# Kernel tuning notes

Hardware: AMD Instinct MI355X
Metric: run time of the kernel (lower is better)

## Reference

```python
import jax, jax.numpy as jnp
import numpy as np

N, NUM_CLASSES, FEAT_DIM = 32768, 395, 512


def setup_inputs() -> dict:
    key = jax.random.key(0)
    k1, k2, k3, k4 = jax.random.split(key, 4)
    modal1_inputs = jax.random.normal(k1, (N, FEAT_DIM), dtype=jnp.float32)
    modal2_inputs = jax.random.normal(k2, (N, FEAT_DIM), dtype=jnp.float32)
    targets = jax.random.randint(k3, (N,), 0, NUM_CLASSES)
    # learned centers parameter: torch.rand -> uniform [0, 1)
    centers = jax.random.uniform(k4, (NUM_CLASSES, FEAT_DIM), dtype=jnp.float32)
    return {
        "modal1_inputs": modal1_inputs,
        "modal2_inputs": modal2_inputs,
        "centers": centers,
        "targets": targets,
    }


def _smooth_l1(a, b):
    # SmoothL1Loss with default beta=1.0, reduction='mean'
    d = jnp.abs(a - b)
    return jnp.mean(jnp.where(d < 1.0, 0.5 * d * d, d - 0.5))


def reference(modal1_inputs, modal2_inputs, centers, targets):
    num_classes = centers.shape[0]
    # Per-label mean (the original O(N^2) loop is exactly a segment mean
    # gathered back per sample).
    ones = jnp.ones((targets.shape[0],), dtype=modal1_inputs.dtype)
    counts = jax.ops.segment_sum(ones, targets, num_segments=num_classes)
    counts = jnp.maximum(counts, 1.0)  # empty classes never gathered
    sum1 = jax.ops.segment_sum(modal1_inputs, targets, num_segments=num_classes)
    sum2 = jax.ops.segment_sum(modal2_inputs, targets, num_segments=num_classes)
    centersR = (sum1 / counts[:, None])[targets]  # [N, D]
    centersT = (sum2 / counts[:, None])[targets]  # [N, D]
    gathered_centers = centers[targets]           # [N, D]
    loss = _smooth_l1(centersR, gathered_centers) + _smooth_l1(centersT, gathered_centers)
    return loss
```

## Files before the change

kernel.cpp:

```cpp
#include <hip/hip_runtime.h>

#define NS 32768
#define NC 395
#define FD 512
#define SPLITS 4

__device__ int   g_hist[NC];
__device__ int   g_offs[NC];
__device__ int   g_cursor[NC];
__device__ float g_countsf[NC];
__device__ int   g_order[NS];
__device__ float g_partial[SPLITS * 2 * NC * FD];

__global__ void hist_scan_kernel(const int* __restrict__ targets,
                                 float* __restrict__ out) {
    __shared__ int lhist[NC];
    __shared__ int sc[512];
    int t = threadIdx.x;
    for (int i = t; i < NC; i += 1024) lhist[i] = 0;
    __syncthreads();
    for (int i = t; i < NS; i += 1024) atomicAdd(&lhist[targets[i]], 1);
    __syncthreads();
    if (t < 512) sc[t] = (t < NC) ? lhist[t] : 0;
    __syncthreads();
    for (int off = 1; off < 512; off <<= 1) {
        int v = 0;
        if (t < 512 && t >= off) v = sc[t - off];
        __syncthreads();
        if (t < 512) sc[t] += v;
        __syncthreads();
    }
    if (t < NC) {
        int cnt = lhist[t];
        int off = sc[t] - cnt;
        g_hist[t]    = cnt;
        g_offs[t]    = off;
        g_cursor[t]  = off;
        g_countsf[t] = (float)cnt;
    }
    if (t == 0) out[0] = 0.0f;
}

__global__ void scatter_kernel(const int* __restrict__ targets) {
    int i = blockIdx.x * blockDim.x + threadIdx.x;
    if (i < NS) {
        int pos = atomicAdd(&g_cursor[targets[i]], 1);
        g_order[pos] = i;
    }
}

__device__ __forceinline__ void f4add(float4& a, const float4 b) {
    a.x += b.x; a.y += b.y; a.z += b.z; a.w += b.w;
}

__global__ void gather_sum_kernel(const float4* __restrict__ m1,
                                  const float4* __restrict__ m2) {
    int c = blockIdx.x >> 2;
    int s = blockIdx.x & 3;
    int tid = threadIdx.x;
    int m = tid >> 7;
    int q = tid & 127;
    const float4* src = m ? m2 : m1;

    int start = g_offs[c];
    int n     = g_hist[c];
    int s0 = start + (n * s) / SPLITS;
    int s1 = start + (n * (s + 1)) / SPLITS;

    float4 a0 = make_float4(0.f, 0.f, 0.f, 0.f);
    float4 a1 = a0, a2 = a0, a3 = a0;

    __shared__ int sidx[256];
    for (int base = s0; base < s1; base += 256) {
        int nn = min(256, s1 - base);
        if (tid < nn) sidx[tid] = g_order[base + tid];
        __syncthreads();
        int j = 0;
        for (; j + 4 <= nn; j += 4) {
            int i0 = sidx[j], i1 = sidx[j + 1], i2 = sidx[j + 2], i3 = sidx[j + 3];
            float4 v0 = src[(size_t)i0 * 128 + q];
            float4 v1 = src[(size_t)i1 * 128 + q];
            float4 v2 = src[(size_t)i2 * 128 + q];
            float4 v3 = src[(size_t)i3 * 128 + q];
            f4add(a0, v0); f4add(a1, v1); f4add(a2, v2); f4add(a3, v3);
        }
        for (; j < nn; j++) {
            f4add(a0, src[(size_t)sidx[j] * 128 + q]);
        }
        __syncthreads();
    }
    f4add(a0, a1); f4add(a2, a3); f4add(a0, a2);

    float4* dst = reinterpret_cast<float4*>(g_partial);
    dst[(((size_t)s * 2 + m) * NC + c) * 128 + q] = a0;
}

__device__ __forceinline__ float smooth_l1(float d) {
    d = fabsf(d);
    return d < 1.0f ? 0.5f * d * d : d - 0.5f;
}

__global__ void loss_kernel(const float* __restrict__ centers,
                            float* __restrict__ out) {
    int gid = blockIdx.x * blockDim.x + threadIdx.x;
    float val = 0.0f;
    if (gid < NC * FD) {
        int c = gid >> 9;
        float cnt = g_countsf[c];
        if (cnt > 0.0f) {
            float sum1 = 0.0f, sum2 = 0.0f;
            #pragma unroll
            for (int s = 0; s < SPLITS; s++) {
                sum1 += g_partial[((s * 2 + 0) * NC) * FD + gid];
                sum2 += g_partial[((s * 2 + 1) * NC) * FD + gid];
            }
            float ctr = centers[gid];
            float inv = 1.0f / cnt;
            float f1 = smooth_l1(sum1 * inv - ctr);
            float f2 = smooth_l1(sum2 * inv - ctr);
            val = cnt * (f1 + f2);
        }
    }
    for (int off = 32; off > 0; off >>= 1)
        val += __shfl_down(val, off, 64);
    __shared__ float wsum[4];
    int lane = threadIdx.x & 63;
    int wid = threadIdx.x >> 6;
    if (lane == 0) wsum[wid] = val;
    __syncthreads();
    if (threadIdx.x == 0) {
        float s = wsum[0] + wsum[1] + wsum[2] + wsum[3];
        atomicAdd(out, s * 5.9604644775390625e-08f);
    }
}

extern "C" void kernel_launch(void* const* d_in, const int* in_sizes, int n_in,
                              void* d_out, int out_size, void* d_ws, size_t ws_size,
                              hipStream_t stream) {
    const float4* m1 = (const float4*)d_in[0];
    const float4* m2 = (const float4*)d_in[1];
    const float* centers = (const float*)d_in[2];
    const int* targets = (const int*)d_in[3];
    float* out = (float*)d_out;

    hist_scan_kernel<<<1, 1024, 0, stream>>>(targets, out);
    scatter_kernel<<<(NS + 255) / 256, 256, 0, stream>>>(targets);
    gather_sum_kernel<<<NC * SPLITS, 256, 0, stream>>>(m1, m2);
    loss_kernel<<<(NC * FD + 255) / 256, 256, 0, stream>>>(centers, out);
}
```

Measured before the change: 197.9 us.

## Parallelize histogram across blocks and double gather splits per class

The single-block histogram over all targets is split into a multi-block partial histogram kernel, followed by a separate scan kernel that sums the per-block partials and computes the class offsets. The gather-sum kernel now uses eight splits per class instead of four, putting more blocks in flight while the inputs are streamed. The cost is one extra kernel launch, a larger partial buffer, and more partial sums to read in the loss kernel.

```diff
diff --git a/kernel.cpp b/kernel.cpp
--- a/kernel.cpp
+++ b/kernel.cpp
@@ -3,8 +3,11 @@
 #define NS 32768
 #define NC 395
 #define FD 512
-#define SPLITS 4
+#define SPLITS 8
+#define HB 128
+#define HT 256
 
+__device__ int   g_hist_part[HB * NC];
 __device__ int   g_hist[NC];
 __device__ int   g_offs[NC];
 __device__ int   g_cursor[NC];
@@ -12,30 +15,37 @@
 __device__ int   g_order[NS];
 __device__ float g_partial[SPLITS * 2 * NC * FD];
 
-__global__ void hist_scan_kernel(const int* __restrict__ targets,
-                                 float* __restrict__ out) {
-    __shared__ int lhist[NC];
+__global__ void hist_kernel(const int* __restrict__ targets) {
+    __shared__ int lh[NC];
+    int t = threadIdx.x;
+    for (int i = t; i < NC; i += HT) lh[i] = 0;
+    __syncthreads();
+    atomicAdd(&lh[targets[blockIdx.x * HT + t]], 1);
+    __syncthreads();
+    int* slab = &g_hist_part[blockIdx.x * NC];
+    for (int c = t; c < NC; c += HT) slab[c] = lh[c];
+}
+
+__global__ void scan_kernel(float* __restrict__ out) {
     __shared__ int sc[512];
     int t = threadIdx.x;
-    for (int i = t; i < NC; i += 1024) lhist[i] = 0;
-    __syncthreads();
-    for (int i = t; i < NS; i += 1024) atomicAdd(&lhist[targets[i]], 1);
-    __syncthreads();
-    if (t < 512) sc[t] = (t < NC) ? lhist[t] : 0;
+    int cnt = 0;
+    if (t < NC) {
+        #pragma unroll 4
+        for (int p = 0; p < HB; p++) cnt += g_hist_part[p * NC + t];
+    }
+    sc[t] = (t < NC) ? cnt : 0;
     __syncthreads();
     for (int off = 1; off < 512; off <<= 1) {
-        int v = 0;
-        if (t < 512 && t >= off) v = sc[t - off];
+        int v = (t >= off) ? sc[t - off] : 0;
         __syncthreads();
-        if (t < 512) sc[t] += v;
+        sc[t] += v;
         __syncthreads();
     }
     if (t < NC) {
-        int cnt = lhist[t];
-        int off = sc[t] - cnt;
         g_hist[t]    = cnt;
-        g_offs[t]    = off;
-        g_cursor[t]  = off;
+        g_offs[t]    = sc[t] - cnt;
+        g_cursor[t]  = sc[t] - cnt;
         g_countsf[t] = (float)cnt;
     }
     if (t == 0) out[0] = 0.0f;
@@ -55,8 +65,8 @@
 
 __global__ void gather_sum_kernel(const float4* __restrict__ m1,
                                   const float4* __restrict__ m2) {
-    int c = blockIdx.x >> 2;
-    int s = blockIdx.x & 3;
+    int c = blockIdx.x >> 3;
+    int s = blockIdx.x & 7;
     int tid = threadIdx.x;
     int m = tid >> 7;
     int q = tid & 127;
@@ -129,8 +139,8 @@
     if (lane == 0) wsum[wid] = val;
     __syncthreads();
     if (threadIdx.x == 0) {
-        float s = wsum[0] + wsum[1] + wsum[2] + wsum[3];
-        atomicAdd(out, s * 5.9604644775390625e-08f);
+        float sm = wsum[0] + wsum[1] + wsum[2] + wsum[3];
+        atomicAdd(out, sm * 5.9604644775390625e-08f);
     }
 }
 
@@ -143,7 +153,8 @@
     const int* targets = (const int*)d_in[3];
     float* out = (float*)d_out;
 
-    hist_scan_kernel<<<1, 1024, 0, stream>>>(targets, out);
+    hist_kernel<<<HB, HT, 0, stream>>>(targets);
+    scan_kernel<<<1, 512, 0, stream>>>(out);
     scatter_kernel<<<(NS + 255) / 256, 256, 0, stream>>>(targets);
     gather_sum_kernel<<<NC * SPLITS, 256, 0, stream>>>(m1, m2);
     loss_kernel<<<(NC * FD + 255) / 256, 256, 0, stream>>>(centers, out);
```

After: 194.5 us. No clear change (-1.8%).

## Fuse class bucketing into gather kernel and drop histogram/scatter passes

Applied to the files above, without the earlier changes.

Removes the single-block histogram/scan kernel and the atomic scatter kernel. Each gather block now scans its own fixed chunk of targets, collects the indices of its class into shared memory, and sums the matching rows. It also writes per-split counts, which the loss kernel adds up. Splits go from 4 to 8. This cuts two launches and a serial single-block pass, at the cost of every block redundantly scanning targets (read from L2) and using a larger shared buffer.

```diff
diff --git a/kernel.cpp b/kernel.cpp
--- a/kernel.cpp
+++ b/kernel.cpp
@@ -3,96 +3,67 @@
 #define NS 32768
 #define NC 395
 #define FD 512
-#define SPLITS 4
+#define SPLITS 8
+#define CHUNK (NS / SPLITS)
+#define TPB 256
 
-__device__ int   g_hist[NC];
-__device__ int   g_offs[NC];
-__device__ int   g_cursor[NC];
-__device__ float g_countsf[NC];
-__device__ int   g_order[NS];
 __device__ float g_partial[SPLITS * 2 * NC * FD];
-
-__global__ void hist_scan_kernel(const int* __restrict__ targets,
-                                 float* __restrict__ out) {
-    __shared__ int lhist[NC];
-    __shared__ int sc[512];
-    int t = threadIdx.x;
-    for (int i = t; i < NC; i += 1024) lhist[i] = 0;
-    __syncthreads();
-    for (int i = t; i < NS; i += 1024) atomicAdd(&lhist[targets[i]], 1);
-    __syncthreads();
-    if (t < 512) sc[t] = (t < NC) ? lhist[t] : 0;
-    __syncthreads();
-    for (int off = 1; off < 512; off <<= 1) {
-        int v = 0;
-        if (t < 512 && t >= off) v = sc[t - off];
-        __syncthreads();
-        if (t < 512) sc[t] += v;
-        __syncthreads();
-    }
-    if (t < NC) {
-        int cnt = lhist[t];
-        int off = sc[t] - cnt;
-        g_hist[t]    = cnt;
-        g_offs[t]    = off;
-        g_cursor[t]  = off;
-        g_countsf[t] = (float)cnt;
-    }
-    if (t == 0) out[0] = 0.0f;
-}
-
-__global__ void scatter_kernel(const int* __restrict__ targets) {
-    int i = blockIdx.x * blockDim.x + threadIdx.x;
-    if (i < NS) {
-        int pos = atomicAdd(&g_cursor[targets[i]], 1);
-        g_order[pos] = i;
-    }
-}
+__device__ int   g_pcount[SPLITS * NC];
 
 __device__ __forceinline__ void f4add(float4& a, const float4 b) {
     a.x += b.x; a.y += b.y; a.z += b.z; a.w += b.w;
 }
 
 __global__ void gather_sum_kernel(const float4* __restrict__ m1,
-                                  const float4* __restrict__ m2) {
-    int c = blockIdx.x >> 2;
-    int s = blockIdx.x & 3;
+                                  const float4* __restrict__ m2,
+                                  const int* __restrict__ targets,
+                                  float* __restrict__ out) {
+    int c   = blockIdx.x >> 3;
+    int s   = blockIdx.x & 7;
     int tid = threadIdx.x;
+
+    if (blockIdx.x == 0 && tid == 0) out[0] = 0.0f;
+
+    __shared__ int sidx[CHUNK];
+    __shared__ int scnt;
+    if (tid == 0) scnt = 0;
+    __syncthreads();
+
+    int base = s * CHUNK;
+    #pragma unroll
+    for (int k = 0; k < CHUNK / TPB; k++) {
+        int i = base + k * TPB + tid;
+        if (targets[i] == c) {
+            int p = atomicAdd(&scnt, 1);
+            sidx[p] = i;
+        }
+    }
+    __syncthreads();
+    int cnt = scnt;
+
     int m = tid >> 7;
     int q = tid & 127;
     const float4* src = m ? m2 : m1;
 
-    int start = g_offs[c];
-    int n     = g_hist[c];
-    int s0 = start + (n * s) / SPLITS;
-    int s1 = start + (n * (s + 1)) / SPLITS;
-
     float4 a0 = make_float4(0.f, 0.f, 0.f, 0.f);
     float4 a1 = a0, a2 = a0, a3 = a0;
 
-    __shared__ int sidx[256];
-    for (int base = s0; base < s1; base += 256) {
-        int nn = min(256, s1 - base);
-        if (tid < nn) sidx[tid] = g_order[base + tid];
-        __syncthreads();
-        int j = 0;
-        for (; j + 4 <= nn; j += 4) {
-            int i0 = sidx[j], i1 = sidx[j + 1], i2 = sidx[j + 2], i3 = sidx[j + 3];
-            float4 v0 = src[(size_t)i0 * 128 + q];
-            float4 v1 = src[(size_t)i1 * 128 + q];
-            float4 v2 = src[(size_t)i2 * 128 + q];
-            float4 v3 = src[(size_t)i3 * 128 + q];
-            f4add(a0, v0); f4add(a1, v1); f4add(a2, v2); f4add(a3, v3);
-        }
-        for (; j < nn; j++) {
-            f4add(a0, src[(size_t)sidx[j] * 128 + q]);
-        }
-        __syncthreads();
+    int j = 0;
+    for (; j + 4 <= cnt; j += 4) {
+        int i0 = sidx[j], i1 = sidx[j + 1], i2 = sidx[j + 2], i3 = sidx[j + 3];
+        float4 v0 = src[(size_t)i0 * 128 + q];
+        float4 v1 = src[(size_t)i1 * 128 + q];
+        float4 v2 = src[(size_t)i2 * 128 + q];
+        float4 v3 = src[(size_t)i3 * 128 + q];
+        f4add(a0, v0); f4add(a1, v1); f4add(a2, v2); f4add(a3, v3);
     }
+    for (; j < cnt; j++)
+        f4add(a0, src[(size_t)sidx[j] * 128 + q]);
     f4add(a0, a1); f4add(a2, a3); f4add(a0, a2);
 
     float4* dst = reinterpret_cast<float4*>(g_partial);
     dst[(((size_t)s * 2 + m) * NC + c) * 128 + q] = a0;
+    if (tid == 0) g_pcount[s * NC + c] = cnt;
 }
 
 __device__ __forceinline__ float smooth_l1(float d) {
@@ -106,14 +77,17 @@
     float val = 0.0f;
     if (gid < NC * FD) {
         int c = gid >> 9;
-        float cnt = g_countsf[c];
-        if (cnt > 0.0f) {
+        int icnt = 0;
+        #pragma unroll
+        for (int s = 0; s < SPLITS; s++) icnt += g_pcount[s * NC + c];
+        if (icnt > 0) {
             float sum1 = 0.0f, sum2 = 0.0f;
             #pragma unroll
             for (int s = 0; s < SPLITS; s++) {
                 sum1 += g_partial[((s * 2 + 0) * NC) * FD + gid];
                 sum2 += g_partial[((s * 2 + 1) * NC) * FD + gid];
             }
+            float cnt = (float)icnt;
             float ctr = centers[gid];
             float inv = 1.0f / cnt;
             float f1 = smooth_l1(sum1 * inv - ctr);
@@ -129,8 +103,8 @@
     if (lane == 0) wsum[wid] = val;
     __syncthreads();
     if (threadIdx.x == 0) {
-        float s = wsum[0] + wsum[1] + wsum[2] + wsum[3];
-        atomicAdd(out, s * 5.9604644775390625e-08f);
+        float sm = wsum[0] + wsum[1] + wsum[2] + wsum[3];
+        atomicAdd(out, sm * 5.9604644775390625e-08f);
     }
 }
 
@@ -143,8 +117,6 @@
     const int* targets = (const int*)d_in[3];
     float* out = (float*)d_out;
 
-    hist_scan_kernel<<<1, 1024, 0, stream>>>(targets, out);
-    scatter_kernel<<<(NS + 255) / 256, 256, 0, stream>>>(targets);
-    gather_sum_kernel<<<NC * SPLITS, 256, 0, stream>>>(m1, m2);
+    gather_sum_kernel<<<NC * SPLITS, TPB, 0, stream>>>(m1, m2, targets, out);
     loss_kernel<<<(NC * FD + 255) / 256, 256, 0, stream>>>(centers, out);
 }
```

New measurement: 176.4 us. -10.9%, faster.
